# Kernel optimization log

Measured on AMD Instinct MI355X. Metric: run time of the kernel, lower is better.

The kernel has to match this reference:

```python
import jax, jax.numpy as jnp
import numpy as np

DIM = 128
IND_DIM = 5
HEADS = 4
DIM_HEAD = 32
HIDDEN = HEADS * DIM_HEAD  # 128
SCALE = DIM_HEAD ** -0.5


def setup_inputs() -> dict:
    key = jax.random.key(0)
    ks = jax.random.split(key, 6)
    b, n = 1, 512
    x = jax.random.normal(ks[0], (b, DIM, n), dtype=jnp.float32)
    indicator = jax.random.normal(ks[1], (b, IND_DIM, n, n), dtype=jnp.float32)
    # conv1d kernels with kernel_size=1 are just (out, in) matrices
    w_qkv = jax.random.normal(ks[2], (HIDDEN * 3, DIM), dtype=jnp.float32) * (DIM ** -0.5)
    w_ind = jax.random.normal(ks[3], (HIDDEN * 2, IND_DIM), dtype=jnp.float32) * (IND_DIM ** -0.5)
    w_out = jax.random.normal(ks[4], (DIM, HIDDEN), dtype=jnp.float32) * (HIDDEN ** -0.5)
    b_out = jax.random.normal(ks[5], (DIM,), dtype=jnp.float32) * 0.01
    return {"x": x, "indicator": indicator, "w_qkv": w_qkv,
            "w_ind": w_ind, "w_out": w_out, "b_out": b_out}


def reference(x, indicator, w_qkv, w_ind, w_out, b_out):
    b, c, n = x.shape
    h, dh = HEADS, DIM_HEAD
    # pointwise conv = channel matmul
    qkv = jnp.einsum('oc,bcn->bon', w_qkv, x)  # (b, 3*hidden, n)
    q, k, v = jnp.split(qkv, 3, axis=1)
    q = q.reshape(b, h, dh, n)
    k = k.reshape(b, h, dh, n)
    v = v.reshape(b, h, dh, n)
    ind = jnp.einsum('oc,bcij->boij', w_ind, indicator)  # (b, 2*hidden, n, n)
    ind_q, ind_k = jnp.split(ind, 2, axis=1)
    ind_q = ind_q.reshape(b, h, dh, n, n)
    ind_k = ind_k.reshape(b, h, dh, n, n)
    qq = (q[..., :, None] + ind_q) * SCALE        # (b, h, dh, n, n)
    kk = k[..., None, :] + ind_k                   # (b, h, dh, n, n)
    sim = jnp.einsum('bhdij,bhdij->bhij', qq, kk)  # (b, h, n, n)
    attn = jax.nn.softmax(sim, axis=-1)
    out = jnp.einsum('bhij,bhdj->bhdi', attn, v)   # (b, h, dh, n)
    out = out.reshape(b, h * dh, n)
    return jnp.einsum('oc,bcn->bon', w_out, out) + b_out[None, :, None]
```

## Files before the change

### kernel.cpp

```cpp
#include <hip/hip_runtime.h>
#include <hip/hip_fp16.h>
#include <math.h>

#define N      512
#define DIMC   128
#define HEADS  4
#define DH     32
#define INDC   5
#define SCALE  0.1767766952966369f

#define QKV_ROWS 384
#define AQ_BASE  384
#define AK_BASE  404
#define TOT_ROWS 424
#define NROW_BLK (TOT_ROWS / 4)

#define MHS_F    (TOT_ROWS * N / 2)
#define WOUTT_F  (MHS_F + 128)
#define ATT_F    (WOUTT_F + DIMC * DIMC)

__global__ __launch_bounds__(256) void pre_kernel(const float* __restrict__ w_qkv,
                                                  const float* __restrict__ w_ind,
                                                  const float* __restrict__ x,
                                                  const float* __restrict__ w_out,
                                                  float* __restrict__ ws) {
    const int bx = blockIdx.x;
    const int t  = threadIdx.x;
    __half* rows  = (__half*)ws;
    float* MhS    = ws + MHS_F;
    float* w_outT = ws + WOUTT_F;

    if (bx == NROW_BLK) {
        if (blockIdx.y != 0) return;
        if (t < HEADS * INDC * INDC) {
            const int h = t / 25, idx = t % 25, c = idx / 5, cc = idx % 5;
            float acc = 0.f;
            for (int d = 0; d < DH; ++d)
                acc = fmaf(w_ind[(h * DH + d) * INDC + c],
                           w_ind[(DIMC + h * DH + d) * INDC + cc], acc);
            MhS[h * 32 + idx] = acc;
        }
        for (int idx = t; idx < DIMC * DIMC; idx += 256) {
            const int o = idx >> 7, c = idx & 127;
            w_outT[c * DIMC + o] = w_out[idx];
        }
        return;
    }

    __shared__ float ws2[4 * DIMC];
    const int o0 = bx * 4;
    for (int idx = t; idx < 4 * DIMC; idx += 256) {
        const int r = idx & 3, m = idx >> 2;
        const int row = o0 + r;
        float val;
        if (row < QKV_ROWS) {
            val = w_qkv[row * DIMC + m];
        } else if (row < AK_BASE) {
            const int rr = row - AQ_BASE, h = rr / INDC, c = rr % INDC;
            float acc = 0.f;
            for (int d = 0; d < DH; ++d)
                acc = fmaf(w_qkv[(h * DH + d) * DIMC + m],
                           w_ind[(DIMC + h * DH + d) * INDC + c], acc);
            val = acc;
        } else {
            const int rr = row - AK_BASE, h = rr / INDC, c = rr % INDC;
            float acc = 0.f;
            for (int d = 0; d < DH; ++d)
                acc = fmaf(w_qkv[(DIMC + h * DH + d) * DIMC + m],
                           w_ind[(h * DH + d) * INDC + c], acc);
            val = acc;
        }
        ws2[m * 4 + r] = val;
    }
    __syncthreads();

    const int i = blockIdx.y * 256 + t;
    float acc[4] = {0.f, 0.f, 0.f, 0.f};
#pragma unroll 8
    for (int c = 0; c < DIMC; ++c) {
        const float xv = x[c * N + i];
        const float4 wv = *(const float4*)(ws2 + c * 4);
        acc[0] = fmaf(wv.x, xv, acc[0]);
        acc[1] = fmaf(wv.y, xv, acc[1]);
        acc[2] = fmaf(wv.z, xv, acc[2]);
        acc[3] = fmaf(wv.w, xv, acc[3]);
    }
#pragma unroll
    for (int r = 0; r < 4; ++r) rows[(o0 + r) * N + i] = __float2half(acc[r]);
}

__global__ __launch_bounds__(256) void attn_kernel(const float* __restrict__ ws_c,
                                                   const float* __restrict__ ind,
                                                   float* __restrict__ ws_w) {
    const int i0   = blockIdx.x * 2;
    const int h    = blockIdx.y;
    const int t    = threadIdx.x;
    const int lane = t & 63;
    const int wave = t >> 6;

    const __half* rows  = (const __half*)ws_c;
    const float* MhS    = ws_c + MHS_F;
    float* att          = ws_w + ATT_F;

    const __half* q  = rows;
    const __half* Aq = rows + 3 * DIMC * N;

    __shared__ float qs[2][DH];
    __shared__ float aqs[2][INDC];
    __shared__ float ms[INDC * INDC];
    __shared__ float ps[2][N];
    __shared__ float red4[2][2][4];
    __shared__ float attv[2][DH];

    if (t < DH)            qs[0][t]      = __half2float(q[(h * DH + t) * N + i0]);
    else if (t < 2 * DH)   qs[1][t - DH] = __half2float(q[(h * DH + t - DH) * N + i0 + 1]);
    else if (t < 2 * DH + INDC)
        aqs[0][t - 2 * DH] = __half2float(Aq[(h * INDC + t - 2 * DH) * N + i0]);
    else if (t < 2 * DH + 2 * INDC)
        aqs[1][t - 2 * DH - INDC] = __half2float(Aq[(h * INDC + t - 2 * DH - INDC) * N + i0 + 1]);
    else if (t >= 96 && t < 96 + 25)
        ms[t - 96] = MhS[h * 32 + (t - 96)];
    __syncthreads();

    float2 ic0[INDC], ic1[INDC];
#pragma unroll
    for (int c = 0; c < INDC; ++c) {
        ic0[c] = ((const float2*)(ind + (c * N + i0) * N))[t];
        ic1[c] = ((const float2*)(ind + (c * N + i0 + 1) * N))[t];
    }

    const __half2* k2  = (const __half2*)(rows + DIMC * N);
    const __half2* Ak2 = (const __half2*)(rows + (3 * DIMC + HEADS * INDC) * N);

    float2 qk0 = {0.f, 0.f}, qk1 = {0.f, 0.f};
#pragma unroll
    for (int d = 0; d < DH; ++d) {
        const float2 kv = __half22float2(k2[(h * DH + d) * 256 + t]);
        const float q0 = qs[0][d], q1 = qs[1][d];
        qk0.x = fmaf(q0, kv.x, qk0.x); qk0.y = fmaf(q0, kv.y, qk0.y);
        qk1.x = fmaf(q1, kv.x, qk1.x); qk1.y = fmaf(q1, kv.y, qk1.y);
    }
    float2 lin0 = {0.f, 0.f}, lin1 = {0.f, 0.f};
#pragma unroll
    for (int c = 0; c < INDC; ++c) {
        const float2 akv = __half22float2(Ak2[(h * INDC + c) * 256 + t]);
        const float a0 = aqs[0][c], a1 = aqs[1][c];
        lin0.x = fmaf(a0 + akv.x, ic0[c].x, lin0.x);
        lin0.y = fmaf(a0 + akv.y, ic0[c].y, lin0.y);
        lin1.x = fmaf(a1 + akv.x, ic1[c].x, lin1.x);
        lin1.y = fmaf(a1 + akv.y, ic1[c].y, lin1.y);
    }
    float2 qd0 = {0.f, 0.f}, qd1 = {0.f, 0.f};
#pragma unroll
    for (int c = 0; c < INDC; ++c) {
        float2 t0 = {0.f, 0.f}, t1 = {0.f, 0.f};
#pragma unroll
        for (int cc = 0; cc < INDC; ++cc) {
            const float mv = ms[c * INDC + cc];
            t0.x = fmaf(mv, ic0[cc].x, t0.x); t0.y = fmaf(mv, ic0[cc].y, t0.y);
            t1.x = fmaf(mv, ic1[cc].x, t1.x); t1.y = fmaf(mv, ic1[cc].y, t1.y);
        }
        qd0.x = fmaf(ic0[c].x, t0.x, qd0.x); qd0.y = fmaf(ic0[c].y, t0.y, qd0.y);
        qd1.x = fmaf(ic1[c].x, t1.x, qd1.x); qd1.y = fmaf(ic1[c].y, t1.y, qd1.y);
    }
    const float s0x = SCALE * (qk0.x + lin0.x + qd0.x);
    const float s0y = SCALE * (qk0.y + lin0.y + qd0.y);
    const float s1x = SCALE * (qk1.x + lin1.x + qd1.x);
    const float s1y = SCALE * (qk1.y + lin1.y + qd1.y);

    float m0 = fmaxf(s0x, s0y), m1 = fmaxf(s1x, s1y);
#pragma unroll
    for (int off = 32; off; off >>= 1) {
        m0 = fmaxf(m0, __shfl_down(m0, off, 64));
        m1 = fmaxf(m1, __shfl_down(m1, off, 64));
    }
    if (lane == 0) { red4[0][0][wave] = m0; red4[0][1][wave] = m1; }
    __syncthreads();
    m0 = fmaxf(fmaxf(red4[0][0][0], red4[0][0][1]), fmaxf(red4[0][0][2], red4[0][0][3]));
    m1 = fmaxf(fmaxf(red4[0][1][0], red4[0][1][1]), fmaxf(red4[0][1][2], red4[0][1][3]));
    const float e0x = __expf(s0x - m0), e0y = __expf(s0y - m0);
    const float e1x = __expf(s1x - m1), e1y = __expf(s1y - m1);
    float su0 = e0x + e0y, su1 = e1x + e1y;
#pragma unroll
    for (int off = 32; off; off >>= 1) {
        su0 += __shfl_down(su0, off, 64);
        su1 += __shfl_down(su1, off, 64);
    }
    __syncthreads();
    if (lane == 0) { red4[1][0][wave] = su0; red4[1][1][wave] = su1; }
    __syncthreads();
    su0 = (red4[1][0][0] + red4[1][0][1]) + (red4[1][0][2] + red4[1][0][3]);
    su1 = (red4[1][1][0] + red4[1][1][1]) + (red4[1][1][2] + red4[1][1][3]);
    const float r0 = 1.f / su0, r1 = 1.f / su1;
    ((float2*)&ps[0][0])[t] = make_float2(e0x * r0, e0y * r0);
    ((float2*)&ps[1][0])[t] = make_float2(e1x * r1, e1y * r1);
    __syncthreads();

    {
        float acc0[8], acc1[8];
#pragma unroll
        for (int dd = 0; dd < 8; ++dd) { acc0[dd] = 0.f; acc1[dd] = 0.f; }
        const float2* ps0 = (const float2*)&ps[0][0];
        const float2* ps1 = (const float2*)&ps[1][0];
        const __half2* v2 = (const __half2*)(rows + 2 * DIMC * N);
        for (int s = 0; s < 4; ++s) {
            const float2 p0 = ps0[lane + 64 * s];
            const float2 p1 = ps1[lane + 64 * s];
#pragma unroll
            for (int dd = 0; dd < 8; ++dd) {
                const float2 vv =
                    __half22float2(v2[(h * DH + wave * 8 + dd) * 256 + lane + 64 * s]);
                acc0[dd] = fmaf(p0.x, vv.x, fmaf(p0.y, vv.y, acc0[dd]));
                acc1[dd] = fmaf(p1.x, vv.x, fmaf(p1.y, vv.y, acc1[dd]));
            }
        }
#pragma unroll
        for (int dd = 0; dd < 8; ++dd) {
            float a0 = acc0[dd], a1 = acc1[dd];
#pragma unroll
            for (int off = 32; off; off >>= 1) {
                a0 += __shfl_down(a0, off, 64);
                a1 += __shfl_down(a1, off, 64);
            }
            if (lane == 0) { attv[0][wave * 8 + dd] = a0; attv[1][wave * 8 + dd] = a1; }
        }
    }
    __syncthreads();

    if (t < 2 * DH) {
        const int ii = t >> 5, d = t & 31;
        att[(i0 + ii) * DIMC + h * DH + d] = attv[ii][d];
    }
}

__global__ __launch_bounds__(128) void outproj_kernel(const float* __restrict__ ws,
                                                      const float* __restrict__ b_out,
                                                      float* __restrict__ out) {
    const int i = blockIdx.x;
    const int t = threadIdx.x;
    const float* w_outT = ws + WOUTT_F;
    const float* att    = ws + ATT_F;
    __shared__ float av[DIMC];
    av[t] = att[i * DIMC + t];
    __syncthreads();
    float acc = 0.f;
#pragma unroll 8
    for (int c = 0; c < DIMC; ++c)
        acc = fmaf(w_outT[c * DIMC + t], av[c], acc);
    out[t * N + i] = acc + b_out[t];
}

extern "C" void kernel_launch(void* const* d_in, const int* in_sizes, int n_in,
                              void* d_out, int out_size, void* d_ws, size_t ws_size,
                              hipStream_t stream) {
    const float* x         = (const float*)d_in[0];
    const float* indicator = (const float*)d_in[1];
    const float* w_qkv     = (const float*)d_in[2];
    const float* w_ind     = (const float*)d_in[3];
    const float* w_out     = (const float*)d_in[4];
    const float* b_out     = (const float*)d_in[5];
    float* out = (float*)d_out;
    float* ws  = (float*)d_ws;

    pre_kernel<<<dim3(NROW_BLK + 1, 2), 256, 0, stream>>>(w_qkv, w_ind, x, w_out, ws);
    attn_kernel<<<dim3(N / 2, HEADS), 256, 0, stream>>>(ws, indicator, ws);
    outproj_kernel<<<N, 128, 0, stream>>>(ws, b_out, out);
}
```

Measured before the change: 103.4 us.

## Assign one query row per wavefront in attention kernel, drop block-level syncs

The attention kernel now maps each wavefront to a single query row, so each block handles 4 rows instead of 2, and each lane handles 8 keys. Softmax reductions become pure wavefront shuffles, with no shared-memory reduction and no __syncthreads. Loads switch to 16-byte vectors, q is broadcast by shuffle, and the P·V product gives one d per lane with a two-half split. This removes block barriers and shared-memory traffic but raises register pressure, and it relies on the same wavefront writing and reading its own psh row without a barrier.

```diff
diff --git a/kernel.cpp b/kernel.cpp
--- a/kernel.cpp
+++ b/kernel.cpp
@@ -92,145 +92,115 @@
 __global__ __launch_bounds__(256) void attn_kernel(const float* __restrict__ ws_c,
                                                    const float* __restrict__ ind,
                                                    float* __restrict__ ws_w) {
-    const int i0   = blockIdx.x * 2;
-    const int h    = blockIdx.y;
     const int t    = threadIdx.x;
     const int lane = t & 63;
-    const int wave = t >> 6;
-
-    const __half* rows  = (const __half*)ws_c;
-    const float* MhS    = ws_c + MHS_F;
-    float* att          = ws_w + ATT_F;
+    const int wv   = t >> 6;
+    const int i    = blockIdx.x * 4 + wv;
+    const int h    = blockIdx.y;
+
+    const __half* rows = (const __half*)ws_c;
+    const float*  Mh   = ws_c + MHS_F;
+    float*        att  = ws_w + ATT_F;
+
+    __shared__ float psh[4][N];
 
     const __half* q  = rows;
     const __half* Aq = rows + 3 * DIMC * N;
-
-    __shared__ float qs[2][DH];
-    __shared__ float aqs[2][INDC];
-    __shared__ float ms[INDC * INDC];
-    __shared__ float ps[2][N];
-    __shared__ float red4[2][2][4];
-    __shared__ float attv[2][DH];
-
-    if (t < DH)            qs[0][t]      = __half2float(q[(h * DH + t) * N + i0]);
-    else if (t < 2 * DH)   qs[1][t - DH] = __half2float(q[(h * DH + t - DH) * N + i0 + 1]);
-    else if (t < 2 * DH + INDC)
-        aqs[0][t - 2 * DH] = __half2float(Aq[(h * INDC + t - 2 * DH) * N + i0]);
-    else if (t < 2 * DH + 2 * INDC)
-        aqs[1][t - 2 * DH - INDC] = __half2float(Aq[(h * INDC + t - 2 * DH - INDC) * N + i0 + 1]);
-    else if (t >= 96 && t < 96 + 25)
-        ms[t - 96] = MhS[h * 32 + (t - 96)];
-    __syncthreads();
-
-    float2 ic0[INDC], ic1[INDC];
+    const float qreg = __half2float(q[(h * DH + (lane & 31)) * N + i]);
+    float aq[INDC];
+#pragma unroll
+    for (int c = 0; c < INDC; ++c)
+        aq[c] = __half2float(Aq[(h * INDC + c) * N + i]);
+    float M[INDC * INDC];
+#pragma unroll
+    for (int p = 0; p < INDC * INDC; ++p) M[p] = Mh[h * 32 + p];
+
+    float ic[INDC][8];
 #pragma unroll
     for (int c = 0; c < INDC; ++c) {
-        ic0[c] = ((const float2*)(ind + (c * N + i0) * N))[t];
-        ic1[c] = ((const float2*)(ind + (c * N + i0 + 1) * N))[t];
-    }
-
-    const __half2* k2  = (const __half2*)(rows + DIMC * N);
-    const __half2* Ak2 = (const __half2*)(rows + (3 * DIMC + HEADS * INDC) * N);
-
-    float2 qk0 = {0.f, 0.f}, qk1 = {0.f, 0.f};
+        const float4* ip = (const float4*)(ind + (c * N + i) * N);
+        *(float4*)&ic[c][0] = ip[lane * 2];
+        *(float4*)&ic[c][4] = ip[lane * 2 + 1];
+    }
+
+    float s[8] = {0.f, 0.f, 0.f, 0.f, 0.f, 0.f, 0.f, 0.f};
+    const float4* k4 = (const float4*)(rows + DIMC * N);
 #pragma unroll
     for (int d = 0; d < DH; ++d) {
-        const float2 kv = __half22float2(k2[(h * DH + d) * 256 + t]);
-        const float q0 = qs[0][d], q1 = qs[1][d];
-        qk0.x = fmaf(q0, kv.x, qk0.x); qk0.y = fmaf(q0, kv.y, qk0.y);
-        qk1.x = fmaf(q1, kv.x, qk1.x); qk1.y = fmaf(q1, kv.y, qk1.y);
-    }
-    float2 lin0 = {0.f, 0.f}, lin1 = {0.f, 0.f};
+        const float qd = __shfl(qreg, d, 64);
+        const float4 kv = k4[(h * DH + d) * 64 + lane];
+        const __half2* kh = (const __half2*)&kv;
+#pragma unroll
+        for (int p = 0; p < 4; ++p) {
+            const float2 kf = __half22float2(kh[p]);
+            s[p * 2 + 0] = fmaf(qd, kf.x, s[p * 2 + 0]);
+            s[p * 2 + 1] = fmaf(qd, kf.y, s[p * 2 + 1]);
+        }
+    }
+    const float4* ak4 = (const float4*)(rows + (3 * DIMC + HEADS * INDC) * N);
 #pragma unroll
     for (int c = 0; c < INDC; ++c) {
-        const float2 akv = __half22float2(Ak2[(h * INDC + c) * 256 + t]);
-        const float a0 = aqs[0][c], a1 = aqs[1][c];
-        lin0.x = fmaf(a0 + akv.x, ic0[c].x, lin0.x);
-        lin0.y = fmaf(a0 + akv.y, ic0[c].y, lin0.y);
-        lin1.x = fmaf(a1 + akv.x, ic1[c].x, lin1.x);
-        lin1.y = fmaf(a1 + akv.y, ic1[c].y, lin1.y);
-    }
-    float2 qd0 = {0.f, 0.f}, qd1 = {0.f, 0.f};
-#pragma unroll
-    for (int c = 0; c < INDC; ++c) {
-        float2 t0 = {0.f, 0.f}, t1 = {0.f, 0.f};
-#pragma unroll
-        for (int cc = 0; cc < INDC; ++cc) {
-            const float mv = ms[c * INDC + cc];
-            t0.x = fmaf(mv, ic0[cc].x, t0.x); t0.y = fmaf(mv, ic0[cc].y, t0.y);
-            t1.x = fmaf(mv, ic1[cc].x, t1.x); t1.y = fmaf(mv, ic1[cc].y, t1.y);
-        }
-        qd0.x = fmaf(ic0[c].x, t0.x, qd0.x); qd0.y = fmaf(ic0[c].y, t0.y, qd0.y);
-        qd1.x = fmaf(ic1[c].x, t1.x, qd1.x); qd1.y = fmaf(ic1[c].y, t1.y, qd1.y);
-    }
-    const float s0x = SCALE * (qk0.x + lin0.x + qd0.x);
-    const float s0y = SCALE * (qk0.y + lin0.y + qd0.y);
-    const float s1x = SCALE * (qk1.x + lin1.x + qd1.x);
-    const float s1y = SCALE * (qk1.y + lin1.y + qd1.y);
-
-    float m0 = fmaxf(s0x, s0y), m1 = fmaxf(s1x, s1y);
-#pragma unroll
-    for (int off = 32; off; off >>= 1) {
-        m0 = fmaxf(m0, __shfl_down(m0, off, 64));
-        m1 = fmaxf(m1, __shfl_down(m1, off, 64));
-    }
-    if (lane == 0) { red4[0][0][wave] = m0; red4[0][1][wave] = m1; }
-    __syncthreads();
-    m0 = fmaxf(fmaxf(red4[0][0][0], red4[0][0][1]), fmaxf(red4[0][0][2], red4[0][0][3]));
-    m1 = fmaxf(fmaxf(red4[0][1][0], red4[0][1][1]), fmaxf(red4[0][1][2], red4[0][1][3]));
-    const float e0x = __expf(s0x - m0), e0y = __expf(s0y - m0);
-    const float e1x = __expf(s1x - m1), e1y = __expf(s1y - m1);
-    float su0 = e0x + e0y, su1 = e1x + e1y;
-#pragma unroll
-    for (int off = 32; off; off >>= 1) {
-        su0 += __shfl_down(su0, off, 64);
-        su1 += __shfl_down(su1, off, 64);
-    }
-    __syncthreads();
-    if (lane == 0) { red4[1][0][wave] = su0; red4[1][1][wave] = su1; }
-    __syncthreads();
-    su0 = (red4[1][0][0] + red4[1][0][1]) + (red4[1][0][2] + red4[1][0][3]);
-    su1 = (red4[1][1][0] + red4[1][1][1]) + (red4[1][1][2] + red4[1][1][3]);
-    const float r0 = 1.f / su0, r1 = 1.f / su1;
-    ((float2*)&ps[0][0])[t] = make_float2(e0x * r0, e0y * r0);
-    ((float2*)&ps[1][0])[t] = make_float2(e1x * r1, e1y * r1);
-    __syncthreads();
-
-    {
-        float acc0[8], acc1[8];
-#pragma unroll
-        for (int dd = 0; dd < 8; ++dd) { acc0[dd] = 0.f; acc1[dd] = 0.f; }
-        const float2* ps0 = (const float2*)&ps[0][0];
-        const float2* ps1 = (const float2*)&ps[1][0];
-        const __half2* v2 = (const __half2*)(rows + 2 * DIMC * N);
-        for (int s = 0; s < 4; ++s) {
-            const float2 p0 = ps0[lane + 64 * s];
-            const float2 p1 = ps1[lane + 64 * s];
-#pragma unroll
-            for (int dd = 0; dd < 8; ++dd) {
-                const float2 vv =
-                    __half22float2(v2[(h * DH + wave * 8 + dd) * 256 + lane + 64 * s]);
-                acc0[dd] = fmaf(p0.x, vv.x, fmaf(p0.y, vv.y, acc0[dd]));
-                acc1[dd] = fmaf(p1.x, vv.x, fmaf(p1.y, vv.y, acc1[dd]));
-            }
-        }
-#pragma unroll
-        for (int dd = 0; dd < 8; ++dd) {
-            float a0 = acc0[dd], a1 = acc1[dd];
-#pragma unroll
-            for (int off = 32; off; off >>= 1) {
-                a0 += __shfl_down(a0, off, 64);
-                a1 += __shfl_down(a1, off, 64);
-            }
-            if (lane == 0) { attv[0][wave * 8 + dd] = a0; attv[1][wave * 8 + dd] = a1; }
-        }
-    }
-    __syncthreads();
-
-    if (t < 2 * DH) {
-        const int ii = t >> 5, d = t & 31;
-        att[(i0 + ii) * DIMC + h * DH + d] = attv[ii][d];
-    }
+        const float4 av = ak4[(h * INDC + c) * 64 + lane];
+        const __half2* ah = (const __half2*)&av;
+#pragma unroll
+        for (int p = 0; p < 4; ++p) {
+            const float2 af = __half22float2(ah[p]);
+            s[p * 2 + 0] = fmaf(aq[c] + af.x, ic[c][p * 2 + 0], s[p * 2 + 0]);
+            s[p * 2 + 1] = fmaf(aq[c] + af.y, ic[c][p * 2 + 1], s[p * 2 + 1]);
+        }
+    }
+#pragma unroll
+    for (int j = 0; j < 8; ++j) {
+        float acc = 0.f;
+#pragma unroll
+        for (int c = 0; c < INDC; ++c) {
+            float tc = 0.f;
+#pragma unroll
+            for (int cc = 0; cc < INDC; ++cc)
+                tc = fmaf(M[c * INDC + cc], ic[cc][j], tc);
+            acc = fmaf(ic[c][j], tc, acc);
+        }
+        s[j] = SCALE * (s[j] + acc);
+    }
+
+    float m = s[0];
+#pragma unroll
+    for (int j = 1; j < 8; ++j) m = fmaxf(m, s[j]);
+#pragma unroll
+    for (int off = 32; off; off >>= 1) m = fmaxf(m, __shfl_xor(m, off, 64));
+    float e[8], sum = 0.f;
+#pragma unroll
+    for (int j = 0; j < 8; ++j) { e[j] = __expf(s[j] - m); sum += e[j]; }
+#pragma unroll
+    for (int off = 32; off; off >>= 1) sum += __shfl_xor(sum, off, 64);
+    const float rs = 1.f / sum;
+#pragma unroll
+    for (int j = 0; j < 8; ++j) e[j] *= rs;
+
+    *(float4*)&psh[wv][lane * 8]     = make_float4(e[0], e[1], e[2], e[3]);
+    *(float4*)&psh[wv][lane * 8 + 4] = make_float4(e[4], e[5], e[6], e[7]);
+
+    const int d = lane & 31, half = lane >> 5;
+    const float4* v4 = (const float4*)(rows + 2 * DIMC * N);
+    const float4* pf = (const float4*)&psh[wv][0];
+    float acc = 0.f;
+#pragma unroll
+    for (int kk = 0; kk < 32; ++kk) {
+        const float4 vv = v4[(h * DH + d) * 64 + half * 32 + kk];
+        const float4 p0 = pf[half * 64 + kk * 2];
+        const float4 p1 = pf[half * 64 + kk * 2 + 1];
+        const __half2* vh = (const __half2*)&vv;
+        const float2 f0 = __half22float2(vh[0]);
+        const float2 f1 = __half22float2(vh[1]);
+        const float2 f2 = __half22float2(vh[2]);
+        const float2 f3 = __half22float2(vh[3]);
+        acc = fmaf(p0.x, f0.x, acc); acc = fmaf(p0.y, f0.y, acc);
+        acc = fmaf(p0.z, f1.x, acc); acc = fmaf(p0.w, f1.y, acc);
+        acc = fmaf(p1.x, f2.x, acc); acc = fmaf(p1.y, f2.y, acc);
+        acc = fmaf(p1.z, f3.x, acc); acc = fmaf(p1.w, f3.y, acc);
+    }
+    acc += __shfl_xor(acc, 32, 64);
+    if (lane < 32) att[i * DIMC + h * DH + lane] = acc;
 }
 
 __global__ __launch_bounds__(128) void outproj_kernel(const float* __restrict__ ws,
@@ -263,6 +233,6 @@
     float* ws  = (float*)d_ws;
 
     pre_kernel<<<dim3(NROW_BLK + 1, 2), 256, 0, stream>>>(w_qkv, w_ind, x, w_out, ws);
-    attn_kernel<<<dim3(N / 2, HEADS), 256, 0, stream>>>(ws, indicator, ws);
+    attn_kernel<<<dim3(N / 4, HEADS), 256, 0, stream>>>(ws, indicator, ws);
     outproj_kernel<<<N, 128, 0, stream>>>(ws, b_out, out);
 }
```

Result: no change. 101.6 us (-1.8%).
